# Optimization experiments

Hardware: AMD Instinct MI355X
Metric: run time of the kernel (lower is better)

The kernel has to match this reference:

```python
import jax, jax.numpy as jnp
import numpy as np

B, OBS, TASK = 65536, 512, 128
D, M, N = 64, 32, 4  # embedding dim, module width, modules per layer


def setup_inputs() -> dict:
    key = jax.random.key(0)
    ks = jax.random.split(key, 16)

    def w(k, shape):
        fan_in = shape[-2]
        return jax.random.normal(k, shape, jnp.float32) * np.float32(np.sqrt(2.0 / fan_in))

    z = lambda *s: jnp.zeros(s, jnp.float32)
    return dict(
        obs=jax.random.normal(ks[0], (B, OBS), jnp.float32),
        task=jax.random.normal(ks[1], (B, TASK), jnp.float32),
        Ws1=w(ks[2], (OBS, D)), bs1=z(D),
        Ws2=w(ks[3], (D, D)), bs2=z(D),
        Wt=w(ks[4], (TASK, D)), bt=z(D),
        Wa0=w(ks[5], (D, N * N)), ba0=z(N * N),
        Wa1=w(ks[6], (D, N * N)), ba1=z(N * N),
        Wc0=w(ks[7], (N * N, D)), bc0=z(D),
        Wc1=w(ks[8], (2 * N * N, D)), bc1=z(D),
        We0=w(ks[9], (N, D, M)), be0=z(N, M),
        We1=w(ks[10], (N, M, M)), be1=z(N, M),
        We2=w(ks[11], (N, M, M)), be2=z(N, M),
    )


def reference(obs, task, Ws1, bs1, Ws2, bs2, Wt, bt, Wa0, ba0, Wa1, ba1,
              Wc0, bc0, Wc1, bc1, We0, be0, We1, be1, We2, be2):
    relu = jax.nn.relu
    # base encoders
    s = relu(relu(obs @ Ws1 + bs1) @ Ws2 + bs2)          # [B, D]
    t = relu(task @ Wt + bt)                              # [B, D]
    r0 = s * t                                            # first routing inputs [B, D]
    prev = jnp.broadcast_to(s[None], (N,) + s.shape)      # [N, B, D] (state emb fed to all layer-0 modules)

    # routing layer 0 -> 1
    a0 = jax.nn.softmax((r0 @ Wa0 + ba0).reshape(-1, N, N), axis=-1)   # [B, N_next, N_prev]
    m = relu(jnp.einsum('nbi,nio->nbo', prev, We0) + be0[:, None, :])  # [N, B, M] expert outputs
    prev = jnp.einsum('bij,jbd->ibd', a0, m)                           # [N, B, M] attention-combined
    r = relu((a0.reshape(-1, N * N) @ Wc0 + bc0) * r0)                 # updated routing inputs

    # routing layer 1 -> 2
    a1 = jax.nn.softmax((r @ Wa1 + ba1).reshape(-1, N, N), axis=-1)
    m = relu(jnp.einsum('nbi,nio->nbo', prev, We1) + be1[:, None, :])
    prev = jnp.einsum('bij,jbd->ibd', a1, m)
    attn_cat = jnp.concatenate([a0.reshape(-1, N * N), a1.reshape(-1, N * N)], axis=-1)
    r = relu((attn_cat @ Wc1 + bc1) * r0)  # computed as in original (unused afterward)

    # final module layer, plain sum over modules
    m = relu(jnp.einsum('nbi,nio->nbo', prev, We2) + be2[:, None, :])  # [N, B, M]
    return relu(m.sum(axis=0))                                          # [B, M]
```

## Files before the change

### kernel.cpp

```cpp
#include <hip/hip_runtime.h>
#include <hip/hip_bf16.h>


using f32x4 = __attribute__((ext_vector_type(4))) float;
using h16x4 = __attribute__((ext_vector_type(4))) _Float16;
using u32x4 = __attribute__((ext_vector_type(4))) unsigned int;
using u32x2 = __attribute__((ext_vector_type(2))) unsigned int;

#define MFMA16(a, b, c) __builtin_amdgcn_mfma_f32_16x16x16f16((a), (b), (c), 0, 0, 0)

__device__ __forceinline__ short h_bits(float f) {
  _Float16 h = (_Float16)f;
  return __builtin_bit_cast(short, h);
}
__device__ __forceinline__ float h2f(unsigned short b) {
  return (float)__builtin_bit_cast(_Float16, b);
}

__device__ __forceinline__ void dma16(const void* g, char* l) {
  __builtin_amdgcn_global_load_lds(
      (const __attribute__((address_space(1))) unsigned int*)g,
      (__attribute__((address_space(3))) unsigned int*)l, 16, 0, 0);
}

__global__ void sm_convert_v10(
    const float* __restrict__ Ws1, const float* __restrict__ Ws2, const float* __restrict__ Wt,
    const float* __restrict__ Wa0, const float* __restrict__ Wa1, const float* __restrict__ Wc0,
    const float* __restrict__ We0, const float* __restrict__ We1, const float* __restrict__ We2,
    const float* __restrict__ bs1, const float* __restrict__ bs2, const float* __restrict__ bt,
    const float* __restrict__ ba0, const float* __restrict__ ba1, const float* __restrict__ bc0,
    const float* __restrict__ be0, const float* __restrict__ be1, const float* __restrict__ be2,
    short* __restrict__ wsh, float* __restrict__ biasf) {
  int d = blockIdx.x * 256 + threadIdx.x;
  if (d < 64512) {
    float v;
    if (d < 32768) {
      int kk   = d & 3;
      int ntip = (d >> 2) & 1;
      int p    = (d >> 3) & 15;
      int q    = (d >> 7) & 3;
      int pair = (d >> 9) & 1;
      int kb2  = (d >> 10) & 1;
      int c    = d >> 11;
      int k = c * 32 + kb2 * 16 + q * 4 + kk;
      int o = pair * 32 + ntip * 16 + p;
      v = Ws1[k * 64 + o];
    }
    else if (d < 36864) { int r = d - 32768, o = r >> 6, k = r & 63;   v = Ws2[k * 64 + o]; }
    else if (d < 45056) {
      int r = d - 36864;
      int kk   = r & 3;
      int ntip = (r >> 2) & 1;
      int p    = (r >> 3) & 15;
      int q    = (r >> 7) & 3;
      int pair = (r >> 9) & 1;
      int kb2  = (r >> 10) & 1;
      int c    = r >> 11;
      int k = c * 32 + kb2 * 16 + q * 4 + kk;
      int o = pair * 32 + ntip * 16 + p;
      v = Wt[k * 64 + o];
    }
    else if (d < 46080) { int r = d - 45056, o = r >> 6, k = r & 63;   v = Wa0[k * 16 + o]; }
    else if (d < 47104) { int r = d - 46080, o = r >> 6, k = r & 63;   v = Wa1[k * 16 + o]; }
    else if (d < 48128) { int r = d - 47104, o = r >> 4, k = r & 15;   v = Wc0[k * 64 + o]; }
    else if (d < 56320) { int r = d - 48128, n = r >> 11, o = (r >> 6) & 31, i = r & 63; v = We0[n * 2048 + i * 32 + o]; }
    else if (d < 60416) { int r = d - 56320, n = r >> 10, o = (r >> 5) & 31, i = r & 31; v = We1[n * 1024 + i * 32 + o]; }
    else                { int r = d - 60416, n = r >> 10, o = (r >> 5) & 31, i = r & 31; v = We2[n * 1024 + i * 32 + o]; }
    wsh[d] = h_bits(v);
  } else if (d < 65184) {
    int r = d - 64512;
    float v;
    if      (r < 64)  v = bs1[r];
    else if (r < 128) v = bs2[r - 64];
    else if (r < 192) v = bt[r - 128];
    else if (r < 208) v = ba0[r - 192];
    else if (r < 224) v = ba1[r - 208];
    else if (r < 288) v = bc0[r - 224];
    else if (r < 416) v = be0[r - 288];
    else if (r < 544) v = be1[r - 416];
    else              v = be2[r - 544];
    biasf[r] = v;
  }
}

__global__ __launch_bounds__(256) void sm_k1_v10(
    const float* __restrict__ obs, const float* __restrict__ task,
    const short* __restrict__ wsh, const float* __restrict__ biasf,
    unsigned* __restrict__ sr) {
  const int tid  = threadIdx.x;
  const int wave = tid >> 6;
  const int lane = tid & 63;
  const int q    = lane >> 4;
  const int p    = lane & 15;
  const int lrow = wave * 16;
  const int wgrow  = blockIdx.x * 64;
  const int rowblk = wgrow + lrow;

  __shared__ __align__(16) char lds[33280];
  char* x_lds = lds;
  char* ring  = lds + 8704;

  const short* Bp1  = wsh;
  const short* Ws2T = wsh + 32768;
  const short* WtP  = wsh + 36864;
  const float* bs1 = biasf;        const float* bs2 = biasf + 64;
  const float* bt  = biasf + 128;

  const f32x4 z4 = {0.f, 0.f, 0.f, 0.f};

  auto stx  = [&](int row, int col, float v) { *(short*)(x_lds + row * 136 + col * 2) = h_bits(v); };
  auto ldx4 = [&](int row, int k0) -> h16x4 { return *(const h16x4*)(x_lds + row * 136 + k0 * 2); };
  auto ldb  = [&](const short* W, int off) -> h16x4 { return *(const h16x4*)(W + off); };
  auto cvtA = [&](const u32x4& u) -> h16x4 {
    float4 v = __builtin_bit_cast(float4, u);
    h16x4 a;
    a[0] = (_Float16)v.x; a[1] = (_Float16)v.y;
    a[2] = (_Float16)v.z; a[3] = (_Float16)v.w;
    return a;
  };
  auto lo2 = [&](const u32x4& u) -> h16x4 { return __builtin_bit_cast(h16x4, (u32x2){u[0], u[1]}); };
  auto hi2 = [&](const u32x4& u) -> h16x4 { return __builtin_bit_cast(h16x4, (u32x2){u[2], u[3]}); };

  auto stageA = [&](const float* base, int rowlen, int k0, int buf) {
#pragma unroll
    for (int j = 0; j < 2; ++j) {
      int f = j * 256 + wave * 64 + lane;
      int row = f >> 3;
      int cl = (f & 7) ^ (row & 7);
      dma16(base + (size_t)(wgrow + row) * rowlen + k0 + cl * 4,
            ring + buf * 12288 + j * 4096 + wave * 1024);
    }
  };
  auto stageB = [&](const short* bsrc, int c, int buf) {
    dma16((const char*)bsrc + c * 4096 + (wave * 64 + lane) * 16,
          ring + buf * 12288 + 8192 + wave * 1024);
  };
  auto lda_ = [&](int buf, int kb2) -> u32x4 {
    return *(const u32x4*)(ring + buf * 12288 + (lrow + p) * 128 +
                           (((kb2 * 4 + q) ^ (p & 7)) * 16));
  };
  auto ldbs = [&](int buf, int kb2, int pair) -> u32x4 {
    return *(const u32x4*)(ring + buf * 12288 + 8192 + kb2 * 2048 + pair * 1024 + lane * 16);
  };

  f32x4 accX[4] = {z4, z4, z4, z4};
  {
    stageA(obs, 512, 0, 0); stageB(Bp1, 0, 0);
    for (int c = 0; c < 16; ++c) {
      asm volatile("s_waitcnt vmcnt(0)" ::: "memory");
      __builtin_amdgcn_s_barrier();
      __builtin_amdgcn_sched_barrier(0);
      if (c + 1 < 16) {
        stageA(obs, 512, (c + 1) * 32, (c + 1) & 1);
        stageB(Bp1, c + 1, (c + 1) & 1);
      }
      __builtin_amdgcn_sched_barrier(0);
      const int buf = c & 1;
#pragma unroll
      for (int kb2 = 0; kb2 < 2; ++kb2) {
        h16x4 a = cvtA(lda_(buf, kb2));
        u32x4 B0 = ldbs(buf, kb2, 0);
        u32x4 B1 = ldbs(buf, kb2, 1);
        accX[0] = MFMA16(a, lo2(B0), accX[0]);
        accX[1] = MFMA16(a, hi2(B0), accX[1]);
        accX[2] = MFMA16(a, lo2(B1), accX[2]);
        accX[3] = MFMA16(a, hi2(B1), accX[3]);
      }
    }
  }

  stageA(task, 128, 0, 0); stageB(WtP, 0, 0);

#pragma unroll
  for (int nt = 0; nt < 4; ++nt) {
    float bias = bs1[nt * 16 + p];
#pragma unroll
    for (int r = 0; r < 4; ++r)
      stx(lrow + 4 * q + r, nt * 16 + p, fmaxf(accX[nt][r] + bias, 0.f));
  }

  f32x4 accS[4] = {z4, z4, z4, z4};
#pragma unroll
  for (int kb = 0; kb < 4; ++kb) {
    h16x4 a = ldx4(lrow + p, kb * 16 + q * 4);
#pragma unroll
    for (int nt = 0; nt < 4; ++nt)
      accS[nt] = MFMA16(a, ldb(Ws2T, (nt * 16 + p) * 64 + kb * 16 + q * 4), accS[nt]);
  }
  float sf[4][4];
#pragma unroll
  for (int nt = 0; nt < 4; ++nt) {
    float bias = bs2[nt * 16 + p];
#pragma unroll
    for (int r = 0; r < 4; ++r) sf[nt][r] = fmaxf(accS[nt][r] + bias, 0.f);
  }

  f32x4 accT[4] = {z4, z4, z4, z4};
  {
    for (int c = 0; c < 4; ++c) {
      asm volatile("s_waitcnt vmcnt(0)" ::: "memory");
      __builtin_amdgcn_s_barrier();
      __builtin_amdgcn_sched_barrier(0);
      if (c + 1 < 4) {
        stageA(task, 128, (c + 1) * 32, (c + 1) & 1);
        stageB(WtP, c + 1, (c + 1) & 1);
      }
      __builtin_amdgcn_sched_barrier(0);
      const int buf = c & 1;
#pragma unroll
      for (int kb2 = 0; kb2 < 2; ++kb2) {
        h16x4 a = cvtA(lda_(buf, kb2));
        u32x4 B0 = ldbs(buf, kb2, 0);
        u32x4 B1 = ldbs(buf, kb2, 1);
        accT[0] = MFMA16(a, lo2(B0), accT[0]);
        accT[1] = MFMA16(a, hi2(B0), accT[1]);
        accT[2] = MFMA16(a, lo2(B1), accT[2]);
        accT[3] = MFMA16(a, hi2(B1), accT[3]);
      }
    }
  }

#pragma unroll
  for (int nt = 0; nt < 4; ++nt) {
    float bias = bt[nt * 16 + p];
#pragma unroll
    for (int r = 0; r < 4; ++r) {
      float tv = fmaxf(accT[nt][r] + bias, 0.f);
      float r0 = sf[nt][r] * tv;
      unsigned pk = (unsigned)(unsigned short)h_bits(sf[nt][r]) |
                    ((unsigned)(unsigned short)h_bits(r0) << 16);
      sr[(size_t)(rowblk + 4 * q + r) * 64 + nt * 16 + p] = pk;
    }
  }
}

__global__ __launch_bounds__(256) void sm_k2_v10(
    const unsigned* __restrict__ sr, const short* __restrict__ wsh,
    const float* __restrict__ biasf, float* __restrict__ out) {
  const int tid  = threadIdx.x;
  const int wave = tid >> 6;
  const int lane = tid & 63;
  const int q    = lane >> 4;
  const int p    = lane & 15;
  const int lrow = wave * 16;
  const int rowblk = blockIdx.x * 64 + lrow;

  __shared__ __align__(16) char lds[20480];
  char* x_lds = lds;
  char* a_lds = lds + 8704;
  char* p_lds = lds;

  const short* Wa0T = wsh + 45056;
  const short* Wa1T = wsh + 46080;
  const short* Wc0T = wsh + 47104;
  const short* We0T = wsh + 48128;
  const short* We1T = wsh + 56320;
  const short* We2T = wsh + 60416;
  const float* ba0 = biasf + 192;  const float* ba1 = biasf + 208;
  const float* bc0 = biasf + 224;  const float* be0 = biasf + 288;
  const float* be1 = biasf + 416;  const float* be2 = biasf + 544;

  const f32x4 z4 = {0.f, 0.f, 0.f, 0.f};

  auto stx  = [&](int row, int col, float v) { *(short*)(x_lds + row * 136 + col * 2) = h_bits(v); };
  auto ldx4 = [&](int row, int k0) -> h16x4 { return *(const h16x4*)(x_lds + row * 136 + k0 * 2); };
  auto ldb  = [&](const short* W, int off) -> h16x4 { return *(const h16x4*)(W + off); };
  auto lo16 = [&](unsigned a, unsigned b) -> unsigned { return (a & 0xffffu) | (b << 16); };
  auto hi16 = [&](unsigned a, unsigned b) -> unsigned { return (a >> 16) | (b & 0xffff0000u); };

  h16x4 sA[4], rA[4];
#pragma unroll
  for (int kb = 0; kb < 4; ++kb) {
    u32x4 v = *(const u32x4*)(sr + (size_t)(rowblk + p) * 64 + kb * 16 + q * 4);
    sA[kb] = __builtin_bit_cast(h16x4, (u32x2){lo16(v[0], v[1]), lo16(v[2], v[3])});
    rA[kb] = __builtin_bit_cast(h16x4, (u32x2){hi16(v[0], v[1]), hi16(v[2], v[3])});
  }
  float r0f[4][4];
#pragma unroll
  for (int nt = 0; nt < 4; ++nt)
#pragma unroll
    for (int r = 0; r < 4; ++r) {
      unsigned v = sr[(size_t)(rowblk + 4 * q + r) * 64 + nt * 16 + p];
      r0f[nt][r] = h2f((unsigned short)(v >> 16));
    }

  float mfr[4][2][4];
#pragma unroll
  for (int n = 0; n < 4; ++n) {
    f32x4 acc[2] = {z4, z4};
#pragma unroll
    for (int kb = 0; kb < 4; ++kb)
#pragma unroll
      for (int nt = 0; nt < 2; ++nt)
        acc[nt] = MFMA16(sA[kb], ldb(We0T, (n * 32 + nt * 16 + p) * 64 + kb * 16 + q * 4), acc[nt]);
#pragma unroll
    for (int nt = 0; nt < 2; ++nt) {
      float bias = be0[n * 32 + nt * 16 + p];
#pragma unroll
      for (int r = 0; r < 4; ++r) mfr[n][nt][r] = fmaxf(acc[nt][r] + bias, 0.f);
    }
  }

  f32x4 accA = z4;
#pragma unroll
  for (int kb = 0; kb < 4; ++kb)
    accA = MFMA16(rA[kb], ldb(Wa0T, p * 64 + kb * 16 + q * 4), accA);
  float a0v[4];
  {
    float bias = ba0[p];
#pragma unroll
    for (int r = 0; r < 4; ++r) {
      float v = accA[r] + bias;
      float mx = fmaxf(v, __shfl_xor(v, 1));
      mx = fmaxf(mx, __shfl_xor(mx, 2));
      float e = __expf(v - mx);
      float ssum = e + __shfl_xor(e, 1);
      ssum += __shfl_xor(ssum, 2);
      a0v[r] = e / ssum;
    }
  }
#pragma unroll
  for (int r = 0; r < 4; ++r)
    *(short*)(a_lds + (lrow + 4 * q + r) * 48 + p * 2) = h_bits(a0v[r]);

  float pv[4][2][4];
#pragma unroll
  for (int i = 0; i < 4; ++i)
#pragma unroll
    for (int nt = 0; nt < 2; ++nt)
#pragma unroll
      for (int r = 0; r < 4; ++r) pv[i][nt][r] = 0.f;
  const int sbase = lane & 48;
#pragma unroll
  for (int r = 0; r < 4; ++r) {
#pragma unroll
    for (int c = 0; c < 16; ++c) {
      float av = __shfl(a0v[r], sbase | c);
      pv[c >> 2][0][r] += av * mfr[c & 3][0][r];
      pv[c >> 2][1][r] += av * mfr[c & 3][1][r];
    }
  }

  f32x4 accC[4] = {z4, z4, z4, z4};
  {
    h16x4 a = *(const h16x4*)(a_lds + (lrow + p) * 48 + q * 8);
#pragma unroll
    for (int nt = 0; nt < 4; ++nt)
      accC[nt] = MFMA16(a, ldb(Wc0T, (nt * 16 + p) * 16 + q * 4), accC[nt]);
  }
  float rf[4][4];
#pragma unroll
  for (int nt = 0; nt < 4; ++nt) {
    float bias = bc0[nt * 16 + p];
#pragma unroll
    for (int r = 0; r < 4; ++r)
      rf[nt][r] = fmaxf((accC[nt][r] + bias) * r0f[nt][r], 0.f);
  }
#pragma unroll
  for (int nt = 0; nt < 4; ++nt)
#pragma unroll
    for (int r = 0; r < 4; ++r) stx(lrow + 4 * q + r, nt * 16 + p, rf[nt][r]);

  f32x4 accA1 = z4;
#pragma unroll
  for (int kb = 0; kb < 4; ++kb)
    accA1 = MFMA16(ldx4(lrow + p, kb * 16 + q * 4), ldb(Wa1T, p * 64 + kb * 16 + q * 4), accA1);
  float a1v[4];
  {
    float bias = ba1[p];
#pragma unroll
    for (int r = 0; r < 4; ++r) {
      float v = accA1[r] + bias;
      float mx = fmaxf(v, __shfl_xor(v, 1));
      mx = fmaxf(mx, __shfl_xor(mx, 2));
      float e = __expf(v - mx);
      float ssum = e + __shfl_xor(e, 1);
      ssum += __shfl_xor(ssum, 2);
      a1v[r] = e / ssum;
    }
  }

  __syncthreads();

#pragma unroll
  for (int i = 0; i < 4; ++i)
#pragma unroll
    for (int nt = 0; nt < 2; ++nt)
#pragma unroll
      for (int r = 0; r < 4; ++r)
        *(short*)(p_lds + (i * 64 + lrow + 4 * q + r) * 80 + (nt * 16 + p) * 2) = h_bits(pv[i][nt][r]);

  float m1f[4][2][4];
#pragma unroll
  for (int n = 0; n < 4; ++n) {
    f32x4 acc[2] = {z4, z4};
#pragma unroll
    for (int kb = 0; kb < 2; ++kb) {
      h16x4 a = *(const h16x4*)(p_lds + (n * 64 + lrow + p) * 80 + kb * 32 + q * 8);
#pragma unroll
      for (int nt = 0; nt < 2; ++nt)
        acc[nt] = MFMA16(a, ldb(We1T, (n * 32 + nt * 16 + p) * 32 + kb * 16 + q * 4), acc[nt]);
    }
#pragma unroll
    for (int nt = 0; nt < 2; ++nt) {
      float bias = be1[n * 32 + nt * 16 + p];
#pragma unroll
      for (int r = 0; r < 4; ++r) m1f[n][nt][r] = fmaxf(acc[nt][r] + bias, 0.f);
    }
  }

#pragma unroll
  for (int i = 0; i < 4; ++i)
#pragma unroll
    for (int nt = 0; nt < 2; ++nt)
#pragma unroll
      for (int r = 0; r < 4; ++r) pv[i][nt][r] = 0.f;
#pragma unroll
  for (int r = 0; r < 4; ++r) {
#pragma unroll
    for (int c = 0; c < 16; ++c) {
      float av = __shfl(a1v[r], sbase | c);
      pv[c >> 2][0][r] += av * m1f[c & 3][0][r];
      pv[c >> 2][1][r] += av * m1f[c & 3][1][r];
    }
  }

#pragma unroll
  for (int i = 0; i < 4; ++i)
#pragma unroll
    for (int nt = 0; nt < 2; ++nt)
#pragma unroll
      for (int r = 0; r < 4; ++r)
        *(short*)(p_lds + (i * 64 + lrow + 4 * q + r) * 80 + (nt * 16 + p) * 2) = h_bits(pv[i][nt][r]);

  float of[2][4] = {{0.f, 0.f, 0.f, 0.f}, {0.f, 0.f, 0.f, 0.f}};
#pragma unroll
  for (int n = 0; n < 4; ++n) {
    f32x4 acc[2] = {z4, z4};
#pragma unroll
    for (int kb = 0; kb < 2; ++kb) {
      h16x4 a = *(const h16x4*)(p_lds + (n * 64 + lrow + p) * 80 + kb * 32 + q * 8);
#pragma unroll
      for (int nt = 0; nt < 2; ++nt)
        acc[nt] = MFMA16(a, ldb(We2T, (n * 32 + nt * 16 + p) * 32 + kb * 16 + q * 4), acc[nt]);
    }
#pragma unroll
    for (int nt = 0; nt < 2; ++nt) {
      float bias = be2[n * 32 + nt * 16 + p];
#pragma unroll
      for (int r = 0; r < 4; ++r) of[nt][r] += fmaxf(acc[nt][r] + bias, 0.f);
    }
  }
#pragma unroll
  for (int nt = 0; nt < 2; ++nt)
#pragma unroll
    for (int r = 0; r < 4; ++r) {
      int grow = rowblk + 4 * q + r;
      out[(size_t)grow * 32 + nt * 16 + p] = of[nt][r];
    }
}

__global__ __launch_bounds__(256) void sm_fused_v10fb(
    const float* __restrict__ obs, const float* __restrict__ task,
    const short* __restrict__ wsh, const float* __restrict__ biasf,
    float* __restrict__ out) {
  const int tid  = threadIdx.x;
  const int wave = tid >> 6;
  const int lane = tid & 63;
  const int q    = lane >> 4;
  const int p    = lane & 15;
  const int lrow = wave * 16;
  const int wgrow  = blockIdx.x * 64;
  const int rowblk = wgrow + lrow;

  __shared__ __align__(16) char lds[36352];
  char* x_lds = lds;
  char* a_lds = lds + 8704;
  char* ring  = lds + 11776;
  char* p_lds = lds;

  const short* Bp1  = wsh;
  const short* Ws2T = wsh + 32768;
  const short* WtP  = wsh + 36864;
  const short* Wa0T = wsh + 45056;
  const short* Wa1T = wsh + 46080;
  const short* Wc0T = wsh + 47104;
  const short* We0T = wsh + 48128;
  const short* We1T = wsh + 56320;
  const short* We2T = wsh + 60416;
  const float* bs1 = biasf;        const float* bs2 = biasf + 64;
  const float* bt  = biasf + 128;  const float* ba0 = biasf + 192;
  const float* ba1 = biasf + 208;  const float* bc0 = biasf + 224;
  const float* be0 = biasf + 288;  const float* be1 = biasf + 416;
  const float* be2 = biasf + 544;

  const f32x4 z4 = {0.f, 0.f, 0.f, 0.f};

  auto stx  = [&](int row, int col, float v) { *(short*)(x_lds + row * 136 + col * 2) = h_bits(v); };
  auto ldx4 = [&](int row, int k0) -> h16x4 { return *(const h16x4*)(x_lds + row * 136 + k0 * 2); };
  auto ldb  = [&](const short* W, int off) -> h16x4 { return *(const h16x4*)(W + off); };
  auto cvtA = [&](const u32x4& u) -> h16x4 {
    float4 v = __builtin_bit_cast(float4, u);
    h16x4 a;
    a[0] = (_Float16)v.x; a[1] = (_Float16)v.y;
    a[2] = (_Float16)v.z; a[3] = (_Float16)v.w;
    return a;
  };
  auto lo2 = [&](const u32x4& u) -> h16x4 { return __builtin_bit_cast(h16x4, (u32x2){u[0], u[1]}); };
  auto hi2 = [&](const u32x4& u) -> h16x4 { return __builtin_bit_cast(h16x4, (u32x2){u[2], u[3]}); };

  auto stageA = [&](const float* base, int rowlen, int k0, int buf) {
#pragma unroll
    for (int j = 0; j < 2; ++j) {
      int f = j * 256 + wave * 64 + lane;
      int row = f >> 3;
      int cl = (f & 7) ^ (row & 7);
      dma16(base + (size_t)(wgrow + row) * rowlen + k0 + cl * 4,
            ring + buf * 12288 + j * 4096 + wave * 1024);
    }
  };
  auto stageB = [&](const short* bsrc, int c, int buf) {
    dma16((const char*)bsrc + c * 4096 + (wave * 64 + lane) * 16,
          ring + buf * 12288 + 8192 + wave * 1024);
  };
  auto lda_ = [&](int buf, int kb2) -> u32x4 {
    return *(const u32x4*)(ring + buf * 12288 + (lrow + p) * 128 +
                           (((kb2 * 4 + q) ^ (p & 7)) * 16));
  };
  auto ldbs = [&](int buf, int kb2, int pair) -> u32x4 {
    return *(const u32x4*)(ring + buf * 12288 + 8192 + kb2 * 2048 + pair * 1024 + lane * 16);
  };

  f32x4 accX[4] = {z4, z4, z4, z4};
  {
    stageA(obs, 512, 0, 0); stageB(Bp1, 0, 0);
    for (int c = 0; c < 16; ++c) {
      asm volatile("s_waitcnt vmcnt(0)" ::: "memory");
      __builtin_amdgcn_s_barrier();
      __builtin_amdgcn_sched_barrier(0);
      if (c + 1 < 16) {
        stageA(obs, 512, (c + 1) * 32, (c + 1) & 1);
        stageB(Bp1, c + 1, (c + 1) & 1);
      }
      __builtin_amdgcn_sched_barrier(0);
      const int buf = c & 1;
#pragma unroll
      for (int kb2 = 0; kb2 < 2; ++kb2) {
        h16x4 a = cvtA(lda_(buf, kb2));
        u32x4 B0 = ldbs(buf, kb2, 0);
        u32x4 B1 = ldbs(buf, kb2, 1);
        accX[0] = MFMA16(a, lo2(B0), accX[0]);
        accX[1] = MFMA16(a, hi2(B0), accX[1]);
        accX[2] = MFMA16(a, lo2(B1), accX[2]);
        accX[3] = MFMA16(a, hi2(B1), accX[3]);
      }
    }
  }
  stageA(task, 128, 0, 0); stageB(WtP, 0, 0);
#pragma unroll
  for (int nt = 0; nt < 4; ++nt) {
    float bias = bs1[nt * 16 + p];
#pragma unroll
    for (int r = 0; r < 4; ++r)
      stx(lrow + 4 * q + r, nt * 16 + p, fmaxf(accX[nt][r] + bias, 0.f));
  }
  f32x4 accS[4] = {z4, z4, z4, z4};
#pragma unroll
  for (int kb = 0; kb < 4; ++kb) {
    h16x4 a = ldx4(lrow + p, kb * 16 + q * 4);
#pragma unroll
    for (int nt = 0; nt < 4; ++nt)
      accS[nt] = MFMA16(a, ldb(Ws2T, (nt * 16 + p) * 64 + kb * 16 + q * 4), accS[nt]);
  }
  float sf[4][4];
#pragma unroll
  for (int nt = 0; nt < 4; ++nt) {
    float bias = bs2[nt * 16 + p];
#pragma unroll
    for (int r = 0; r < 4; ++r) sf[nt][r] = fmaxf(accS[nt][r] + bias, 0.f);
  }
#pragma unroll
  for (int nt = 0; nt < 4; ++nt)
#pragma unroll
    for (int r = 0; r < 4; ++r) stx(lrow + 4 * q + r, nt * 16 + p, sf[nt][r]);
  f32x4 accT[4] = {z4, z4, z4, z4};
  {
    for (int c = 0; c < 4; ++c) {
      asm volatile("s_waitcnt vmcnt(0)" ::: "memory");
      __builtin_amdgcn_s_barrier();
      __builtin_amdgcn_sched_barrier(0);
      if (c + 1 < 4) {
        stageA(task, 128, (c + 1) * 32, (c + 1) & 1);
        stageB(WtP, c + 1, (c + 1) & 1);
      }
      __builtin_amdgcn_sched_barrier(0);
      const int buf = c & 1;
#pragma unroll
      for (int kb2 = 0; kb2 < 2; ++kb2) {
        h16x4 a = cvtA(lda_(buf, kb2));
        u32x4 B0 = ldbs(buf, kb2, 0);
        u32x4 B1 = ldbs(buf, kb2, 1);
        accT[0] = MFMA16(a, lo2(B0), accT[0]);
        accT[1] = MFMA16(a, hi2(B0), accT[1]);
        accT[2] = MFMA16(a, lo2(B1), accT[2]);
        accT[3] = MFMA16(a, hi2(B1), accT[3]);
      }
    }
  }
  float r0f[4][4];
#pragma unroll
  for (int nt = 0; nt < 4; ++nt) {
    float bias = bt[nt * 16 + p];
#pragma unroll
    for (int r = 0; r < 4; ++r)
      r0f[nt][r] = sf[nt][r] * fmaxf(accT[nt][r] + bias, 0.f);
  }
  float mfr[4][2][4];
#pragma unroll
  for (int n = 0; n < 4; ++n) {
    f32x4 acc[2] = {z4, z4};
#pragma unroll
    for (int kb = 0; kb < 4; ++kb) {
      h16x4 a = ldx4(lrow + p, kb * 16 + q * 4);
#pragma unroll
      for (int nt = 0; nt < 2; ++nt)
        acc[nt] = MFMA16(a, ldb(We0T, (n * 32 + nt * 16 + p) * 64 + kb * 16 + q * 4), acc[nt]);
    }
#pragma unroll
    for (int nt = 0; nt < 2; ++nt) {
      float bias = be0[n * 32 + nt * 16 + p];
#pragma unroll
      for (int r = 0; r < 4; ++r) mfr[n][nt][r] = fmaxf(acc[nt][r] + bias, 0.f);
    }
  }
#pragma unroll
  for (int nt = 0; nt < 4; ++nt)
#pragma unroll
    for (int r = 0; r < 4; ++r) stx(lrow + 4 * q + r, nt * 16 + p, r0f[nt][r]);
  f32x4 accA = z4;
#pragma unroll
  for (int kb = 0; kb < 4; ++kb)
    accA = MFMA16(ldx4(lrow + p, kb * 16 + q * 4), ldb(Wa0T, p * 64 + kb * 16 + q * 4), accA);
  float a0v[4];
  {
    float bias = ba0[p];
#pragma unroll
    for (int r = 0; r < 4; ++r) {
      float v = accA[r] + bias;
      float mx = fmaxf(v, __shfl_xor(v, 1));
      mx = fmaxf(mx, __shfl_xor(mx, 2));
      float e = __expf(v - mx);
      float ssum = e + __shfl_xor(e, 1);
      ssum += __shfl_xor(ssum, 2);
      a0v[r] = e / ssum;
    }
  }
#pragma unroll
  for (int r = 0; r < 4; ++r)
    *(short*)(a_lds + (lrow + 4 * q + r) * 48 + p * 2) = h_bits(a0v[r]);
  float pv[4][2][4];
#pragma unroll
  for (int i = 0; i < 4; ++i)
#pragma unroll
    for (int nt = 0; nt < 2; ++nt)
#pragma unroll
      for (int r = 0; r < 4; ++r) pv[i][nt][r] = 0.f;
  const int sbase = lane & 48;
#pragma unroll
  for (int r = 0; r < 4; ++r) {
#pragma unroll
    for (int c = 0; c < 16; ++c) {
      float av = __shfl(a0v[r], sbase | c);
      pv[c >> 2][0][r] += av * mfr[c & 3][0][r];
      pv[c >> 2][1][r] += av * mfr[c & 3][1][r];
    }
  }
  f32x4 accC[4] = {z4, z4, z4, z4};
  {
    h16x4 a = *(const h16x4*)(a_lds + (lrow + p) * 48 + q * 8);
#pragma unroll
    for (int nt = 0; nt < 4; ++nt)
      accC[nt] = MFMA16(a, ldb(Wc0T, (nt * 16 + p) * 16 + q * 4), accC[nt]);
  }
  float rf[4][4];
#pragma unroll
  for (int nt = 0; nt < 4; ++nt) {
    float bias = bc0[nt * 16 + p];
#pragma unroll
    for (int r = 0; r < 4; ++r)
      rf[nt][r] = fmaxf((accC[nt][r] + bias) * r0f[nt][r], 0.f);
  }
#pragma unroll
  for (int nt = 0; nt < 4; ++nt)
#pragma unroll
    for (int r = 0; r < 4; ++r) stx(lrow + 4 * q + r, nt * 16 + p, rf[nt][r]);
  f32x4 accA1 = z4;
#pragma unroll
  for (int kb = 0; kb < 4; ++kb)
    accA1 = MFMA16(ldx4(lrow + p, kb * 16 + q * 4), ldb(Wa1T, p * 64 + kb * 16 + q * 4), accA1);
  float a1v[4];
  {
    float bias = ba1[p];
#pragma unroll
    for (int r = 0; r < 4; ++r) {
      float v = accA1[r] + bias;
      float mx = fmaxf(v, __shfl_xor(v, 1));
      mx = fmaxf(mx, __shfl_xor(mx, 2));
      float e = __expf(v - mx);
      float ssum = e + __shfl_xor(e, 1);
      ssum += __shfl_xor(ssum, 2);
      a1v[r] = e / ssum;
    }
  }
  __syncthreads();
#pragma unroll
  for (int i = 0; i < 4; ++i)
#pragma unroll
    for (int nt = 0; nt < 2; ++nt)
#pragma unroll
      for (int r = 0; r < 4; ++r)
        *(short*)(p_lds + (i * 64 + lrow + 4 * q + r) * 80 + (nt * 16 + p) * 2) = h_bits(pv[i][nt][r]);
  float m1f[4][2][4];
#pragma unroll
  for (int n = 0; n < 4; ++n) {
    f32x4 acc[2] = {z4, z4};
#pragma unroll
    for (int kb = 0; kb < 2; ++kb) {
      h16x4 a = *(const h16x4*)(p_lds + (n * 64 + lrow + p) * 80 + kb * 32 + q * 8);
#pragma unroll
      for (int nt = 0; nt < 2; ++nt)
        acc[nt] = MFMA16(a, ldb(We1T, (n * 32 + nt * 16 + p) * 32 + kb * 16 + q * 4), acc[nt]);
    }
#pragma unroll
    for (int nt = 0; nt < 2; ++nt) {
      float bias = be1[n * 32 + nt * 16 + p];
#pragma unroll
      for (int r = 0; r < 4; ++r) m1f[n][nt][r] = fmaxf(acc[nt][r] + bias, 0.f);
    }
  }
#pragma unroll
  for (int i = 0; i < 4; ++i)
#pragma unroll
    for (int nt = 0; nt < 2; ++nt)
#pragma unroll
      for (int r = 0; r < 4; ++r) pv[i][nt][r] = 0.f;
#pragma unroll
  for (int r = 0; r < 4; ++r) {
#pragma unroll
    for (int c = 0; c < 16; ++c) {
      float av = __shfl(a1v[r], sbase | c);
      pv[c >> 2][0][r] += av * m1f[c & 3][0][r];
      pv[c >> 2][1][r] += av * m1f[c & 3][1][r];
    }
  }
#pragma unroll
  for (int i = 0; i < 4; ++i)
#pragma unroll
    for (int nt = 0; nt < 2; ++nt)
#pragma unroll
      for (int r = 0; r < 4; ++r)
        *(short*)(p_lds + (i * 64 + lrow + 4 * q + r) * 80 + (nt * 16 + p) * 2) = h_bits(pv[i][nt][r]);
  float of[2][4] = {{0.f, 0.f, 0.f, 0.f}, {0.f, 0.f, 0.f, 0.f}};
#pragma unroll
  for (int n = 0; n < 4; ++n) {
    f32x4 acc[2] = {z4, z4};
#pragma unroll
    for (int kb = 0; kb < 2; ++kb) {
      h16x4 a = *(const h16x4*)(p_lds + (n * 64 + lrow + p) * 80 + kb * 32 + q * 8);
#pragma unroll
      for (int nt = 0; nt < 2; ++nt)
        acc[nt] = MFMA16(a, ldb(We2T, (n * 32 + nt * 16 + p) * 32 + kb * 16 + q * 4), acc[nt]);
    }
#pragma unroll
    for (int nt = 0; nt < 2; ++nt) {
      float bias = be2[n * 32 + nt * 16 + p];
#pragma unroll
      for (int r = 0; r < 4; ++r) of[nt][r] += fmaxf(acc[nt][r] + bias, 0.f);
    }
  }
#pragma unroll
  for (int nt = 0; nt < 2; ++nt)
#pragma unroll
    for (int r = 0; r < 4; ++r) {
      int grow = rowblk + 4 * q + r;
      out[(size_t)grow * 32 + nt * 16 + p] = of[nt][r];
    }
}

extern "C" void kernel_launch(void* const* d_in, const int* in_sizes, int n_in,
                              void* d_out, int out_size, void* d_ws, size_t ws_size,
                              hipStream_t stream) {
  (void)in_sizes; (void)n_in; (void)out_size;
  const float* obs  = (const float*)d_in[0];
  const float* task = (const float*)d_in[1];
  const float* Ws1 = (const float*)d_in[2];  const float* bs1 = (const float*)d_in[3];
  const float* Ws2 = (const float*)d_in[4];  const float* bs2 = (const float*)d_in[5];
  const float* Wt  = (const float*)d_in[6];  const float* bt  = (const float*)d_in[7];
  const float* Wa0 = (const float*)d_in[8];  const float* ba0 = (const float*)d_in[9];
  const float* Wa1 = (const float*)d_in[10]; const float* ba1 = (const float*)d_in[11];
  const float* Wc0 = (const float*)d_in[12]; const float* bc0 = (const float*)d_in[13];
  const float* We0 = (const float*)d_in[16]; const float* be0 = (const float*)d_in[17];
  const float* We1 = (const float*)d_in[18]; const float* be1 = (const float*)d_in[19];
  const float* We2 = (const float*)d_in[20]; const float* be2 = (const float*)d_in[21];

  short* wsh   = (short*)d_ws;
  float* biasf = (float*)((char*)d_ws + 129040);

  sm_convert_v10<<<dim3(255), dim3(256), 0, stream>>>(
      Ws1, Ws2, Wt, Wa0, Wa1, Wc0, We0, We1, We2,
      bs1, bs2, bt, ba0, ba1, bc0, be0, be1, be2,
      wsh, biasf);

  const size_t need = (size_t)(1 << 20) + (size_t)65536 * 64 * 4;
  if (ws_size >= need) {
    unsigned* sr = (unsigned*)((char*)d_ws + (1 << 20));
    sm_k1_v10<<<dim3(1024), dim3(256), 0, stream>>>(obs, task, wsh, biasf, sr);
    sm_k2_v10<<<dim3(1024), dim3(256), 0, stream>>>(sr, wsh, biasf, (float*)d_out);
  } else {
    sm_fused_v10fb<<<dim3(1024), dim3(256), 0, stream>>>(
        obs, task, wsh, biasf, (float*)d_out);
  }
}
```

Baseline: 75.70 us.

## Run k2 as single-wave blocks and read attention weights from LDS

```diff
diff --git a/kernel.cpp b/kernel.cpp
--- a/kernel.cpp
+++ b/kernel.cpp
@@ -4,6 +4,7 @@
 
 using f32x4 = __attribute__((ext_vector_type(4))) float;
 using h16x4 = __attribute__((ext_vector_type(4))) _Float16;
+using h16x8 = __attribute__((ext_vector_type(8))) _Float16;
 using u32x4 = __attribute__((ext_vector_type(4))) unsigned int;
 using u32x2 = __attribute__((ext_vector_type(2))) unsigned int;
 
@@ -23,7 +24,7 @@
       (__attribute__((address_space(3))) unsigned int*)l, 16, 0, 0);
 }
 
-__global__ void sm_convert_v10(
+__global__ void sm_convert_v11(
     const float* __restrict__ Ws1, const float* __restrict__ Ws2, const float* __restrict__ Wt,
     const float* __restrict__ Wa0, const float* __restrict__ Wa1, const float* __restrict__ Wc0,
     const float* __restrict__ We0, const float* __restrict__ We1, const float* __restrict__ We2,
@@ -83,7 +84,7 @@
   }
 }
 
-__global__ __launch_bounds__(256) void sm_k1_v10(
+__global__ __launch_bounds__(256) void sm_k1_v11(
     const float* __restrict__ obs, const float* __restrict__ task,
     const short* __restrict__ wsh, const float* __restrict__ biasf,
     unsigned* __restrict__ sr) {
@@ -234,21 +235,18 @@
   }
 }
 
-__global__ __launch_bounds__(256) void sm_k2_v10(
+__global__ __launch_bounds__(64, 4) void sm_k2_v11(
     const unsigned* __restrict__ sr, const short* __restrict__ wsh,
     const float* __restrict__ biasf, float* __restrict__ out) {
-  const int tid  = threadIdx.x;
-  const int wave = tid >> 6;
-  const int lane = tid & 63;
+  const int lane = threadIdx.x & 63;
   const int q    = lane >> 4;
   const int p    = lane & 15;
-  const int lrow = wave * 16;
-  const int rowblk = blockIdx.x * 64 + lrow;
-
-  __shared__ __align__(16) char lds[20480];
+  const int rowblk = blockIdx.x * 16;
+
+  __shared__ __align__(16) char lds[8192];
   char* x_lds = lds;
-  char* a_lds = lds + 8704;
-  char* p_lds = lds;
+  char* a_lds = lds + 2176;
+  char* pm_lds = lds + 2944;
 
   const short* Wa0T = wsh + 45056;
   const short* Wa1T = wsh + 46080;
@@ -262,8 +260,6 @@
 
   const f32x4 z4 = {0.f, 0.f, 0.f, 0.f};
 
-  auto stx  = [&](int row, int col, float v) { *(short*)(x_lds + row * 136 + col * 2) = h_bits(v); };
-  auto ldx4 = [&](int row, int k0) -> h16x4 { return *(const h16x4*)(x_lds + row * 136 + k0 * 2); };
   auto ldb  = [&](const short* W, int off) -> h16x4 { return *(const h16x4*)(W + off); };
   auto lo16 = [&](unsigned a, unsigned b) -> unsigned { return (a & 0xffffu) | (b << 16); };
   auto hi16 = [&](unsigned a, unsigned b) -> unsigned { return (a >> 16) | (b & 0xffff0000u); };
@@ -321,29 +317,31 @@
   }
 #pragma unroll
   for (int r = 0; r < 4; ++r)
-    *(short*)(a_lds + (lrow + 4 * q + r) * 48 + p * 2) = h_bits(a0v[r]);
+    *(short*)(a_lds + (4 * q + r) * 48 + p * 2) = h_bits(a0v[r]);
 
   float pv[4][2][4];
 #pragma unroll
-  for (int i = 0; i < 4; ++i)
-#pragma unroll
-    for (int nt = 0; nt < 2; ++nt)
-#pragma unroll
-      for (int r = 0; r < 4; ++r) pv[i][nt][r] = 0.f;
-  const int sbase = lane & 48;
-#pragma unroll
   for (int r = 0; r < 4; ++r) {
-#pragma unroll
-    for (int c = 0; c < 16; ++c) {
-      float av = __shfl(a0v[r], sbase | c);
-      pv[c >> 2][0][r] += av * mfr[c & 3][0][r];
-      pv[c >> 2][1][r] += av * mfr[c & 3][1][r];
+    h16x8 a0lo = *(const h16x8*)(a_lds + (4 * q + r) * 48);
+    h16x8 a0hi = *(const h16x8*)(a_lds + (4 * q + r) * 48 + 16);
+    float av[16];
+#pragma unroll
+    for (int e = 0; e < 8; ++e) { av[e] = (float)a0lo[e]; av[8 + e] = (float)a0hi[e]; }
+#pragma unroll
+    for (int i = 0; i < 4; ++i) {
+      float s0 = 0.f, s1 = 0.f;
+#pragma unroll
+      for (int j = 0; j < 4; ++j) {
+        s0 += av[4 * i + j] * mfr[j][0][r];
+        s1 += av[4 * i + j] * mfr[j][1][r];
+      }
+      pv[i][0][r] = s0; pv[i][1][r] = s1;
     }
   }
 
   f32x4 accC[4] = {z4, z4, z4, z4};
   {
-    h16x4 a = *(const h16x4*)(a_lds + (lrow + p) * 48 + q * 8);
+    h16x4 a = *(const h16x4*)(a_lds + p * 48 + q * 8);
 #pragma unroll
     for (int nt = 0; nt < 4; ++nt)
       accC[nt] = MFMA16(a, ldb(Wc0T, (nt * 16 + p) * 16 + q * 4), accC[nt]);
@@ -359,12 +357,15 @@
 #pragma unroll
   for (int nt = 0; nt < 4; ++nt)
 #pragma unroll
-    for (int r = 0; r < 4; ++r) stx(lrow + 4 * q + r, nt * 16 + p, rf[nt][r]);
+    for (int r = 0; r < 4; ++r)
+      *(short*)(x_lds + (4 * q + r) * 136 + (nt * 16 + p) * 2) = h_bits(rf[nt][r]);
 
   f32x4 accA1 = z4;
 #pragma unroll
-  for (int kb = 0; kb < 4; ++kb)
-    accA1 = MFMA16(ldx4(lrow + p, kb * 16 + q * 4), ldb(Wa1T, p * 64 + kb * 16 + q * 4), accA1);
+  for (int kb = 0; kb < 4; ++kb) {
+    h16x4 a = *(const h16x4*)(x_lds + p * 136 + (kb * 16 + q * 4) * 2);
+    accA1 = MFMA16(a, ldb(Wa1T, p * 64 + kb * 16 + q * 4), accA1);
+  }
   float a1v[4];
   {
     float bias = ba1[p];
@@ -379,8 +380,9 @@
       a1v[r] = e / ssum;
     }
   }
-
-  __syncthreads();
+#pragma unroll
+  for (int r = 0; r < 4; ++r)
+    *(short*)(a_lds + (4 * q + r) * 48 + p * 2) = h_bits(a1v[r]);
 
 #pragma unroll
   for (int i = 0; i < 4; ++i)
@@ -388,7 +390,7 @@
     for (int nt = 0; nt < 2; ++nt)
 #pragma unroll
       for (int r = 0; r < 4; ++r)
-        *(short*)(p_lds + (i * 64 + lrow + 4 * q + r) * 80 + (nt * 16 + p) * 2) = h_bits(pv[i][nt][r]);
+        *(short*)(pm_lds + (i * 16 + 4 * q + r) * 80 + (nt * 16 + p) * 2) = h_bits(pv[i][nt][r]);
 
   float m1f[4][2][4];
 #pragma unroll
@@ -396,7 +398,7 @@
     f32x4 acc[2] = {z4, z4};
 #pragma unroll
     for (int kb = 0; kb < 2; ++kb) {
-      h16x4 a = *(const h16x4*)(p_lds + (n * 64 + lrow + p) * 80 + kb * 32 + q * 8);
+      h16x4 a = *(const h16x4*)(pm_lds + (n * 16 + p) * 80 + kb * 32 + q * 8);
 #pragma unroll
       for (int nt = 0; nt < 2; ++nt)
         acc[nt] = MFMA16(a, ldb(We1T, (n * 32 + nt * 16 + p) * 32 + kb * 16 + q * 4), acc[nt]);
@@ -410,28 +412,31 @@
   }
 
 #pragma unroll
+  for (int r = 0; r < 4; ++r) {
+    h16x8 a1lo = *(const h16x8*)(a_lds + (4 * q + r) * 48);
+    h16x8 a1hi = *(const h16x8*)(a_lds + (4 * q + r) * 48 + 16);
+    float av[16];
+#pragma unroll
+    for (int e = 0; e < 8; ++e) { av[e] = (float)a1lo[e]; av[8 + e] = (float)a1hi[e]; }
+#pragma unroll
+    for (int i = 0; i < 4; ++i) {
+      float s0 = 0.f, s1 = 0.f;
+#pragma unroll
+      for (int j = 0; j < 4; ++j) {
+        s0 += av[4 * i + j] * m1f[j][0][r];
+        s1 += av[4 * i + j] * m1f[j][1][r];
+      }
+      pv[i][0][r] = s0; pv[i][1][r] = s1;
+    }
+  }
+
+#pragma unroll
   for (int i = 0; i < 4; ++i)
 #pragma unroll
     for (int nt = 0; nt < 2; ++nt)
 #pragma unroll
-      for (int r = 0; r < 4; ++r) pv[i][nt][r] = 0.f;
-#pragma unroll
-  for (int r = 0; r < 4; ++r) {
-#pragma unroll
-    for (int c = 0; c < 16; ++c) {
-      float av = __shfl(a1v[r], sbase | c);
-      pv[c >> 2][0][r] += av * m1f[c & 3][0][r];
-      pv[c >> 2][1][r] += av * m1f[c & 3][1][r];
-    }
-  }
-
-#pragma unroll
-  for (int i = 0; i < 4; ++i)
-#pragma unroll
-    for (int nt = 0; nt < 2; ++nt)
-#pragma unroll
       for (int r = 0; r < 4; ++r)
-        *(short*)(p_lds + (i * 64 + lrow + 4 * q + r) * 80 + (nt * 16 + p) * 2) = h_bits(pv[i][nt][r]);
+        *(short*)(pm_lds + (i * 16 + 4 * q + r) * 80 + (nt * 16 + p) * 2) = h_bits(pv[i][nt][r]);
 
   float of[2][4] = {{0.f, 0.f, 0.f, 0.f}, {0.f, 0.f, 0.f, 0.f}};
 #pragma unroll
@@ -439,7 +444,7 @@
     f32x4 acc[2] = {z4, z4};
 #pragma unroll
     for (int kb = 0; kb < 2; ++kb) {
-      h16x4 a = *(const h16x4*)(p_lds + (n * 64 + lrow + p) * 80 + kb * 32 + q * 8);
+      h16x4 a = *(const h16x4*)(pm_lds + (n * 16 + p) * 80 + kb * 32 + q * 8);
 #pragma unroll
       for (int nt = 0; nt < 2; ++nt)
         acc[nt] = MFMA16(a, ldb(We2T, (n * 32 + nt * 16 + p) * 32 + kb * 16 + q * 4), acc[nt]);
@@ -460,7 +465,7 @@
     }
 }
 
-__global__ __launch_bounds__(256) void sm_fused_v10fb(
+__global__ __launch_bounds__(256) void sm_fused_v11fb(
     const float* __restrict__ obs, const float* __restrict__ task,
     const short* __restrict__ wsh, const float* __restrict__ biasf,
     float* __restrict__ out) {
@@ -806,7 +811,7 @@
   short* wsh   = (short*)d_ws;
   float* biasf = (float*)((char*)d_ws + 129040);
 
-  sm_convert_v10<<<dim3(255), dim3(256), 0, stream>>>(
+  sm_convert_v11<<<dim3(255), dim3(256), 0, stream>>>(
       Ws1, Ws2, Wt, Wa0, Wa1, Wc0, We0, We1, We2,
       bs1, bs2, bt, ba0, ba1, bc0, be0, be1, be2,
       wsh, biasf);
@@ -814,10 +819,10 @@
   const size_t need = (size_t)(1 << 20) + (size_t)65536 * 64 * 4;
   if (ws_size >= need) {
     unsigned* sr = (unsigned*)((char*)d_ws + (1 << 20));
-    sm_k1_v10<<<dim3(1024), dim3(256), 0, stream>>>(obs, task, wsh, biasf, sr);
-    sm_k2_v10<<<dim3(1024), dim3(256), 0, stream>>>(sr, wsh, biasf, (float*)d_out);
+    sm_k1_v11<<<dim3(1024), dim3(256), 0, stream>>>(obs, task, wsh, biasf, sr);
+    sm_k2_v11<<<dim3(4096), dim3(64), 0, stream>>>(sr, wsh, biasf, (float*)d_out);
   } else {
-    sm_fused_v10fb<<<dim3(1024), dim3(256), 0, stream>>>(
+    sm_fused_v11fb<<<dim3(1024), dim3(256), 0, stream>>>(
         obs, task, wsh, biasf, (float*)d_out);
   }
 }
```

Result: faster. 73.92 us (-2.4%).
